# Kernel optimization log

Measured on AMD Instinct MI355X. Metric: run time of the kernel, lower is better.

Reference implementation:

```python
import jax, jax.numpy as jnp
import numpy as np

TEMPERATURE = 0.1
NEG_INF = -1e30


def setup_inputs() -> dict:
    key = jax.random.key(0)
    kf, kl = jax.random.split(key)
    N, D = 8192, 128
    features = jax.random.normal(kf, (N, D), dtype=jnp.float32)
    # labels in [-1, 80): -1 marks background rows that are filtered out
    labels = jax.random.randint(kl, (N,), -1, 80)
    return {"features": features, "labels": labels}


def reference(features, labels):
    N = labels.shape[0]
    fg = labels >= 0  # [N]

    # F.normalize(p=2, dim=1): x / max(||x||, eps)
    norm = jnp.maximum(jnp.linalg.norm(features, axis=1, keepdims=True), 1e-12)
    f = features / norm

    sim = jnp.matmul(f, f.T) / TEMPERATURE  # [N, N]

    pair_fg = fg[:, None] & fg[None, :]
    eye = jnp.eye(N, dtype=bool)
    label_eq = labels[:, None] == labels[None, :]
    pos_mask = pair_fg & label_eq & ~eye          # positives (same label, not self)
    all_mask = pair_fg & ~eye                     # pos | neg == everything but self (within fg)

    # row-wise masked max, clamped to [-20, 20] as in the original
    max_sim = jnp.max(jnp.where(all_mask, sim, NEG_INF), axis=1)
    max_sim = jnp.clip(max_sim, -20.0, 20.0)

    e = jnp.exp(sim - max_sim[:, None])           # cos-sim/temp is bounded, no overflow
    pos_sum = jnp.clip(jnp.sum(jnp.where(pos_mask, e, 0.0), axis=1), 1e-6, 1e6)
    all_sum = jnp.clip(jnp.sum(jnp.where(all_mask, e, 0.0), axis=1), 1e-6, 1e6)

    loss_i = jnp.minimum(-jnp.log(pos_sum / all_sum), 10.0)  # clamp(max=10)

    # rows contributing to the mean: fg rows with at least one positive
    valid = fg & (jnp.sum(pos_mask, axis=1) > 0)
    n_valid = jnp.sum(valid)
    mean_loss = jnp.sum(jnp.where(valid, loss_i, 0.0)) / jnp.maximum(n_valid, 1).astype(jnp.float32)

    ok = (jnp.sum(fg) >= 2) & (n_valid > 0)
    return jnp.where(ok, mean_loss, jnp.float32(0.0))
```

## Files before the change

### kernel.cpp

```cpp
#include <hip/hip_runtime.h>

#define N 8192
#define D 128
#define CHUNK 512
#define NCHUNK (N / CHUNK)
#define TILE_IT (CHUNK / 128)

typedef unsigned short u16;
typedef __attribute__((ext_vector_type(8))) __bf16 bf16x8;
typedef __attribute__((ext_vector_type(4))) float f32x4;

#define PREP_SCALE 3.7982889979f

__device__ __forceinline__ u16 f2bf(float x) {
  unsigned u = __float_as_uint(x);
  u += 0x7fff + ((u >> 16) & 1);
  return (u16)(u >> 16);
}
__device__ __forceinline__ float bf2f(u16 h) {
  return __uint_as_float(((unsigned)h) << 16);
}

__global__ __launch_bounds__(256) void cpe_prep(const float* __restrict__ feat,
                                                u16* __restrict__ fhi,
                                                u16* __restrict__ flo,
                                                float* __restrict__ acc3) {
  if (blockIdx.x == 0 && threadIdx.x < 4) acc3[threadIdx.x] = 0.0f;
  const int w = threadIdx.x >> 6, l = threadIdx.x & 63;
  const int row = blockIdx.x * 4 + w;
  const float2 x = *(const float2*)&feat[row * D + l * 2];
  float s = x.x * x.x + x.y * x.y;
#pragma unroll
  for (int sh = 1; sh < 64; sh <<= 1) s += __shfl_xor(s, sh);
  const float inv = PREP_SCALE / fmaxf(sqrtf(s), 1e-12f);
  const float a = x.x * inv, b = x.y * inv;
  const u16 ah = f2bf(a), bh = f2bf(b);
  const u16 al = f2bf(a - bf2f(ah)), bl = f2bf(b - bf2f(bh));
  *(ushort2*)&fhi[row * D + l * 2] = make_ushort2(ah, bh);
  *(ushort2*)&flo[row * D + l * 2] = make_ushort2(al, bl);
}

__global__ __launch_bounds__(256, 2) void cpe_main(
    const u16* __restrict__ fhi, const u16* __restrict__ flo,
    const int* __restrict__ labels, float4* __restrict__ partials) {
  __shared__ __align__(16) u16 Bh[128 * 128];
  __shared__ __align__(16) u16 Bl[128 * 128];
  __shared__ int Lab[CHUNK];
  const int rt = blockIdx.x, cc = blockIdx.y;
  const int tid = threadIdx.x;
  const int w = tid >> 6, l = tid & 63, q = l >> 4, m = l & 15;
  const int r0w = rt * 256 + w * 64;
  const int cbase0 = cc * CHUNK;

  Lab[tid] = labels[cbase0 + tid];
  Lab[tid + 256] = labels[cbase0 + 256 + tid];

  bf16x8 Ah[4][4];
  int labi[4][4];
#pragma unroll
  for (int tr = 0; tr < 4; ++tr) {
    const int row = r0w + tr * 16 + m;
#pragma unroll
    for (int ks = 0; ks < 4; ++ks)
      Ah[tr][ks] = *(const bf16x8*)&fhi[row * D + ks * 32 + q * 8];
#pragma unroll
    for (int v = 0; v < 4; ++v) labi[tr][v] = labels[r0w + tr * 16 + q * 4 + v];
  }

  float mxe[4][4], ps[4][4], as_[4][4];
#pragma unroll
  for (int tr = 0; tr < 4; ++tr)
#pragma unroll
    for (int v = 0; v < 4; ++v) { mxe[tr][v] = 0.f; ps[tr][v] = 0.f; as_[tr][v] = 0.f; }

  for (int it = 0; it < TILE_IT; ++it) {
    const int cbase = cbase0 + it * 128;
    __syncthreads();
#pragma unroll
    for (int n = 0; n < 8; ++n) {
      const int r = w * 32 + n * 4 + q;
      const int c = m ^ (r & 15);
      const u16* gh = &fhi[(size_t)(cbase + r) * D + c * 8];
      const u16* gl = &flo[(size_t)(cbase + r) * D + c * 8];
      __builtin_amdgcn_global_load_lds(
          (const __attribute__((address_space(1))) unsigned*)gh,
          (__attribute__((address_space(3))) unsigned*)&Bh[(w * 512 + n * 64) * 8],
          16, 0, 0);
      __builtin_amdgcn_global_load_lds(
          (const __attribute__((address_space(1))) unsigned*)gl,
          (__attribute__((address_space(3))) unsigned*)&Bl[(w * 512 + n * 64) * 8],
          16, 0, 0);
    }
    __syncthreads();

    for (int ct = 0; ct < 8; ++ct) {
      const int jj = ct * 16 + m;
      f32x4 acc[4];
#pragma unroll
      for (int tr = 0; tr < 4; ++tr) acc[tr] = (f32x4){0.f, 0.f, 0.f, 0.f};
#pragma unroll
      for (int ks = 0; ks < 4; ++ks) {
        const int off = jj * 128 + ((ks * 4 + q) ^ m) * 8;
        const bf16x8 bh = *(const bf16x8*)&Bh[off];
        const bf16x8 bl = *(const bf16x8*)&Bl[off];
#pragma unroll
        for (int tr = 0; tr < 4; ++tr)
          acc[tr] = __builtin_amdgcn_mfma_f32_16x16x32_bf16(Ah[tr][ks], bh, acc[tr], 0, 0, 0);
#pragma unroll
        for (int tr = 0; tr < 4; ++tr)
          acc[tr] = __builtin_amdgcn_mfma_f32_16x16x32_bf16(Ah[tr][ks], bl, acc[tr], 0, 0, 0);
      }
      const int labj = Lab[it * 128 + jj];
      const bool fgj = labj >= 0;
      const int jbase = cbase + ct * 16;
#pragma unroll
      for (int tr = 0; tr < 4; ++tr) {
        if (jbase == r0w + tr * 16) {
#pragma unroll
          for (int v = 0; v < 4; ++v) {
            const float e = exp2f(acc[tr][v]);
            const float em = (fgj && (m != q * 4 + v)) ? e : 0.0f;
            as_[tr][v] += em;
            mxe[tr][v] = fmaxf(mxe[tr][v], em);
            ps[tr][v] += (labj == labi[tr][v]) ? em : 0.0f;
          }
        } else {
#pragma unroll
          for (int v = 0; v < 4; ++v) {
            const float e = exp2f(acc[tr][v]);
            const float em = fgj ? e : 0.0f;
            as_[tr][v] += em;
            mxe[tr][v] = fmaxf(mxe[tr][v], em);
            ps[tr][v] += (labj == labi[tr][v]) ? em : 0.0f;
          }
        }
      }
    }
  }

#pragma unroll
  for (int tr = 0; tr < 4; ++tr)
#pragma unroll
    for (int v = 0; v < 4; ++v) {
      float vm = mxe[tr][v], vp = ps[tr][v], va = as_[tr][v];
#pragma unroll
      for (int s = 1; s < 16; s <<= 1) {
        vm = fmaxf(vm, __shfl_xor(vm, s));
        vp += __shfl_xor(vp, s);
        va += __shfl_xor(va, s);
      }
      if (m == 0)
        partials[(size_t)cc * N + r0w + tr * 16 + q * 4 + v] =
            make_float4(vm, vp, va, 0.f);
    }
}

__global__ __launch_bounds__(256) void cpe_rows(const float4* __restrict__ partials,
                                                const int* __restrict__ labels,
                                                float* __restrict__ acc3,
                                                float* __restrict__ out) {
  const int r = blockIdx.x * 256 + threadIdx.x;
  float mxe = 0.f, ps = 0.f, as_ = 0.f;
#pragma unroll
  for (int c = 0; c < NCHUNK; ++c) {
    const float4 p = partials[(size_t)c * N + r];
    mxe = fmaxf(mxe, p.x); ps += p.y; as_ += p.z;
  }
  const bool fg = labels[r] >= 0;
  const bool valid = fg && (ps > 0.f);
  const float pos = fminf(fmaxf(ps / mxe, 1e-6f), 1e6f);
  const float all = fminf(fmaxf(as_ / mxe, 1e-6f), 1e6f);
  const float loss = fminf(-logf(pos / all), 10.0f);
  float v0 = valid ? loss : 0.f;
  float v1 = valid ? 1.f : 0.f;
  float v2 = fg ? 1.f : 0.f;
#pragma unroll
  for (int s = 1; s < 64; s <<= 1) {
    v0 += __shfl_xor(v0, s); v1 += __shfl_xor(v1, s); v2 += __shfl_xor(v2, s);
  }
  __shared__ float red[3][4];
  const int w = threadIdx.x >> 6, l = threadIdx.x & 63;
  if (l == 0) { red[0][w] = v0; red[1][w] = v1; red[2][w] = v2; }
  __syncthreads();
  if (threadIdx.x == 0) {
    atomicAdd(&acc3[0], red[0][0] + red[0][1] + red[0][2] + red[0][3]);
    atomicAdd(&acc3[1], red[1][0] + red[1][1] + red[1][2] + red[1][3]);
    atomicAdd(&acc3[2], red[2][0] + red[2][1] + red[2][2] + red[2][3]);
    __threadfence();
    const unsigned old = atomicAdd((unsigned*)&acc3[3], 1u);
    if (old == gridDim.x - 1) {
      const float ls = atomicAdd(&acc3[0], 0.0f);
      const float nv = atomicAdd(&acc3[1], 0.0f);
      const float nf = atomicAdd(&acc3[2], 0.0f);
      out[0] = (nf >= 2.0f && nv > 0.0f) ? ls / fmaxf(nv, 1.0f) : 0.0f;
    }
  }
}

extern "C" void kernel_launch(void* const* d_in, const int* in_sizes, int n_in,
                              void* d_out, int out_size, void* d_ws, size_t ws_size,
                              hipStream_t stream) {
  const float* feat = (const float*)d_in[0];
  const int* labels = (const int*)d_in[1];
  float* out = (float*)d_out;
  char* ws = (char*)d_ws;
  u16* fhi = (u16*)ws;
  u16* flo = (u16*)(ws + (size_t)N * D * 2);
  float4* partials = (float4*)(ws + (size_t)N * D * 4);
  float* acc3 = (float*)(ws + (size_t)N * D * 4 + (size_t)NCHUNK * N * 16);

  cpe_prep<<<N / 4, 256, 0, stream>>>(feat, fhi, flo, acc3);
  cpe_main<<<dim3(N / 256, NCHUNK), 256, 0, stream>>>(fhi, flo, labels, partials);
  cpe_rows<<<N / 256, 256, 0, stream>>>(partials, labels, acc3, out);
}
```

Measured before the change: 117.2 us.

## Move lo-part to register A operand, drop row max and masking via zeroed background rows

The hi/lo split correction now puts the low bf16 part on the A side, which is held in registers. Only the high part of B is staged through LDS, halving LDS traffic and the global-to-LDS loads. Background rows are zeroed in the prep kernel, so the masking happens implicitly: each background column adds exp2(0)=1 per row, which is subtracted through a per-chunk count. The self term is subtracted through a stored diagonal exp value. The row max tracking is dropped because the fixed scale keeps the exps bounded, and a native exp2 builtin, float2 partials and a wider prep kernel are added. The risks are the precision loss from subtracting large counts from the sums, and dropping the lo*hi product on the B side in favour of lo(A)*hi(B), which is a different but symmetric approximation.

```diff
diff --git a/kernel.cpp b/kernel.cpp
--- a/kernel.cpp
+++ b/kernel.cpp
@@ -3,14 +3,21 @@
 #define N 8192
 #define D 128
 #define CHUNK 512
-#define NCHUNK (N / CHUNK)
-#define TILE_IT (CHUNK / 128)
+#define NCHUNK 16
+#define TILE_IT 4
+#define PREP_SCALE 3.7982889979f
 
 typedef unsigned short u16;
 typedef __attribute__((ext_vector_type(8))) __bf16 bf16x8;
 typedef __attribute__((ext_vector_type(4))) float f32x4;
 
-#define PREP_SCALE 3.7982889979f
+__device__ __forceinline__ float fast_exp2(float x) {
+#if __has_builtin(__builtin_amdgcn_exp2f)
+  return __builtin_amdgcn_exp2f(x);
+#else
+  return exp2f(x);
+#endif
+}
 
 __device__ __forceinline__ u16 f2bf(float x) {
   unsigned u = __float_as_uint(x);
@@ -22,56 +29,66 @@
 }
 
 __global__ __launch_bounds__(256) void cpe_prep(const float* __restrict__ feat,
+                                                const int* __restrict__ labels,
                                                 u16* __restrict__ fhi,
                                                 u16* __restrict__ flo,
-                                                float* __restrict__ acc3) {
-  if (blockIdx.x == 0 && threadIdx.x < 4) acc3[threadIdx.x] = 0.0f;
-  const int w = threadIdx.x >> 6, l = threadIdx.x & 63;
-  const int row = blockIdx.x * 4 + w;
-  const float2 x = *(const float2*)&feat[row * D + l * 2];
-  float s = x.x * x.x + x.y * x.y;
-#pragma unroll
-  for (int sh = 1; sh < 64; sh <<= 1) s += __shfl_xor(s, sh);
-  const float inv = PREP_SCALE / fmaxf(sqrtf(s), 1e-12f);
-  const float a = x.x * inv, b = x.y * inv;
-  const u16 ah = f2bf(a), bh = f2bf(b);
-  const u16 al = f2bf(a - bf2f(ah)), bl = f2bf(b - bf2f(bh));
-  *(ushort2*)&fhi[row * D + l * 2] = make_ushort2(ah, bh);
-  *(ushort2*)&flo[row * D + l * 2] = make_ushort2(al, bl);
+                                                float* __restrict__ accum) {
+  if (blockIdx.x == 0 && threadIdx.x < 4) accum[threadIdx.x] = 0.0f;
+  const int w = threadIdx.x >> 6, l = threadIdx.x & 63, q = l >> 4, m = l & 15;
+  const int row = (int)blockIdx.x * 16 + w * 4 + q;
+  const int lab = labels[row];
+  const float4 x0 = *(const float4*)&feat[row * D + m * 8];
+  const float4 x1 = *(const float4*)&feat[row * D + m * 8 + 4];
+  float s = x0.x * x0.x + x0.y * x0.y + x0.z * x0.z + x0.w * x0.w +
+            x1.x * x1.x + x1.y * x1.y + x1.z * x1.z + x1.w * x1.w;
+#pragma unroll
+  for (int sh = 1; sh < 16; sh <<= 1) s += __shfl_xor(s, sh);
+  float inv = PREP_SCALE / fmaxf(sqrtf(s), 1e-12f);
+  if (lab < 0) inv = 0.0f;
+  const float a[8] = {x0.x * inv, x0.y * inv, x0.z * inv, x0.w * inv,
+                      x1.x * inv, x1.y * inv, x1.z * inv, x1.w * inv};
+  u16 h[8], lo[8];
+#pragma unroll
+  for (int k = 0; k < 8; ++k) {
+    h[k] = f2bf(a[k]);
+    lo[k] = f2bf(a[k] - bf2f(h[k]));
+  }
+  *(ushort4*)&fhi[row * D + m * 8] = make_ushort4(h[0], h[1], h[2], h[3]);
+  *(ushort4*)&fhi[row * D + m * 8 + 4] = make_ushort4(h[4], h[5], h[6], h[7]);
+  *(ushort4*)&flo[row * D + m * 8] = make_ushort4(lo[0], lo[1], lo[2], lo[3]);
+  *(ushort4*)&flo[row * D + m * 8 + 4] = make_ushort4(lo[4], lo[5], lo[6], lo[7]);
 }
 
 __global__ __launch_bounds__(256, 2) void cpe_main(
     const u16* __restrict__ fhi, const u16* __restrict__ flo,
-    const int* __restrict__ labels, float4* __restrict__ partials) {
+    const int* __restrict__ labels, float2* __restrict__ partials,
+    float* __restrict__ eself) {
   __shared__ __align__(16) u16 Bh[128 * 128];
-  __shared__ __align__(16) u16 Bl[128 * 128];
-  __shared__ int Lab[CHUNK];
   const int rt = blockIdx.x, cc = blockIdx.y;
   const int tid = threadIdx.x;
   const int w = tid >> 6, l = tid & 63, q = l >> 4, m = l & 15;
   const int r0w = rt * 256 + w * 64;
   const int cbase0 = cc * CHUNK;
 
-  Lab[tid] = labels[cbase0 + tid];
-  Lab[tid + 256] = labels[cbase0 + 256 + tid];
-
-  bf16x8 Ah[4][4];
+  bf16x8 Ah[4][4], Al[4][4];
   int labi[4][4];
 #pragma unroll
   for (int tr = 0; tr < 4; ++tr) {
     const int row = r0w + tr * 16 + m;
 #pragma unroll
-    for (int ks = 0; ks < 4; ++ks)
+    for (int ks = 0; ks < 4; ++ks) {
       Ah[tr][ks] = *(const bf16x8*)&fhi[row * D + ks * 32 + q * 8];
+      Al[tr][ks] = *(const bf16x8*)&flo[row * D + ks * 32 + q * 8];
+    }
 #pragma unroll
     for (int v = 0; v < 4; ++v) labi[tr][v] = labels[r0w + tr * 16 + q * 4 + v];
   }
 
-  float mxe[4][4], ps[4][4], as_[4][4];
+  float ps[4][4], as_[4][4], bgc = 0.f;
 #pragma unroll
   for (int tr = 0; tr < 4; ++tr)
 #pragma unroll
-    for (int v = 0; v < 4; ++v) { mxe[tr][v] = 0.f; ps[tr][v] = 0.f; as_[tr][v] = 0.f; }
+    for (int v = 0; v < 4; ++v) { ps[tr][v] = 0.f; as_[tr][v] = 0.f; }
 
   for (int it = 0; it < TILE_IT; ++it) {
     const int cbase = cbase0 + it * 128;
@@ -80,119 +97,118 @@
     for (int n = 0; n < 8; ++n) {
       const int r = w * 32 + n * 4 + q;
       const int c = m ^ (r & 15);
-      const u16* gh = &fhi[(size_t)(cbase + r) * D + c * 8];
-      const u16* gl = &flo[(size_t)(cbase + r) * D + c * 8];
       __builtin_amdgcn_global_load_lds(
-          (const __attribute__((address_space(1))) unsigned*)gh,
-          (__attribute__((address_space(3))) unsigned*)&Bh[(w * 512 + n * 64) * 8],
-          16, 0, 0);
-      __builtin_amdgcn_global_load_lds(
-          (const __attribute__((address_space(1))) unsigned*)gl,
-          (__attribute__((address_space(3))) unsigned*)&Bl[(w * 512 + n * 64) * 8],
+          (const __attribute__((address_space(1))) unsigned*)
+              &fhi[(size_t)(cbase + r) * D + c * 8],
+          (__attribute__((address_space(3))) unsigned*)
+              &Bh[(w * 512 + n * 64) * 8],
           16, 0, 0);
     }
     __syncthreads();
 
     for (int ct = 0; ct < 8; ++ct) {
       const int jj = ct * 16 + m;
+      const int jbase = cbase + ct * 16;
+      const int labj = labels[jbase + m];
       f32x4 acc[4];
 #pragma unroll
       for (int tr = 0; tr < 4; ++tr) acc[tr] = (f32x4){0.f, 0.f, 0.f, 0.f};
 #pragma unroll
       for (int ks = 0; ks < 4; ++ks) {
-        const int off = jj * 128 + ((ks * 4 + q) ^ m) * 8;
-        const bf16x8 bh = *(const bf16x8*)&Bh[off];
-        const bf16x8 bl = *(const bf16x8*)&Bl[off];
+        const bf16x8 bh = *(const bf16x8*)&Bh[jj * 128 + ((ks * 4 + q) ^ m) * 8];
 #pragma unroll
         for (int tr = 0; tr < 4; ++tr)
           acc[tr] = __builtin_amdgcn_mfma_f32_16x16x32_bf16(Ah[tr][ks], bh, acc[tr], 0, 0, 0);
 #pragma unroll
         for (int tr = 0; tr < 4; ++tr)
-          acc[tr] = __builtin_amdgcn_mfma_f32_16x16x32_bf16(Ah[tr][ks], bl, acc[tr], 0, 0, 0);
+          acc[tr] = __builtin_amdgcn_mfma_f32_16x16x32_bf16(Al[tr][ks], bh, acc[tr], 0, 0, 0);
       }
-      const int labj = Lab[it * 128 + jj];
-      const bool fgj = labj >= 0;
-      const int jbase = cbase + ct * 16;
+      bgc += (labj < 0) ? 1.0f : 0.0f;
 #pragma unroll
       for (int tr = 0; tr < 4; ++tr) {
         if (jbase == r0w + tr * 16) {
 #pragma unroll
           for (int v = 0; v < 4; ++v) {
-            const float e = exp2f(acc[tr][v]);
-            const float em = (fgj && (m != q * 4 + v)) ? e : 0.0f;
-            as_[tr][v] += em;
-            mxe[tr][v] = fmaxf(mxe[tr][v], em);
-            ps[tr][v] += (labj == labi[tr][v]) ? em : 0.0f;
+            const float e = fast_exp2(acc[tr][v]);
+            if (m == q * 4 + v) eself[jbase + m] = e;
+            as_[tr][v] += e;
+            ps[tr][v] += (labj == labi[tr][v]) ? e : 0.f;
           }
         } else {
 #pragma unroll
           for (int v = 0; v < 4; ++v) {
-            const float e = exp2f(acc[tr][v]);
-            const float em = fgj ? e : 0.0f;
-            as_[tr][v] += em;
-            mxe[tr][v] = fmaxf(mxe[tr][v], em);
-            ps[tr][v] += (labj == labi[tr][v]) ? em : 0.0f;
+            const float e = fast_exp2(acc[tr][v]);
+            as_[tr][v] += e;
+            ps[tr][v] += (labj == labi[tr][v]) ? e : 0.f;
           }
         }
       }
     }
   }
 
+  float vbg = bgc;
+#pragma unroll
+  for (int s = 1; s < 16; s <<= 1) vbg += __shfl_xor(vbg, s);
 #pragma unroll
   for (int tr = 0; tr < 4; ++tr)
 #pragma unroll
     for (int v = 0; v < 4; ++v) {
-      float vm = mxe[tr][v], vp = ps[tr][v], va = as_[tr][v];
+      float vp = ps[tr][v], va = as_[tr][v];
 #pragma unroll
       for (int s = 1; s < 16; s <<= 1) {
-        vm = fmaxf(vm, __shfl_xor(vm, s));
         vp += __shfl_xor(vp, s);
         va += __shfl_xor(va, s);
       }
       if (m == 0)
         partials[(size_t)cc * N + r0w + tr * 16 + q * 4 + v] =
-            make_float4(vm, vp, va, 0.f);
-    }
-}
-
-__global__ __launch_bounds__(256) void cpe_rows(const float4* __restrict__ partials,
+            make_float2(vp, va - vbg);
+    }
+}
+
+__global__ __launch_bounds__(256) void cpe_rows(const float2* __restrict__ partials,
                                                 const int* __restrict__ labels,
-                                                float* __restrict__ acc3,
+                                                const float* __restrict__ eself,
+                                                float* __restrict__ accum,
                                                 float* __restrict__ out) {
   const int r = blockIdx.x * 256 + threadIdx.x;
-  float mxe = 0.f, ps = 0.f, as_ = 0.f;
+  float ps = 0.f, as_ = 0.f;
 #pragma unroll
   for (int c = 0; c < NCHUNK; ++c) {
-    const float4 p = partials[(size_t)c * N + r];
-    mxe = fmaxf(mxe, p.x); ps += p.y; as_ += p.z;
-  }
-  const bool fg = labels[r] >= 0;
-  const bool valid = fg && (ps > 0.f);
-  const float pos = fminf(fmaxf(ps / mxe, 1e-6f), 1e6f);
-  const float all = fminf(fmaxf(as_ / mxe, 1e-6f), 1e6f);
-  const float loss = fminf(-logf(pos / all), 10.0f);
+    const float2 p = partials[(size_t)c * N + r];
+    ps += p.x;
+    as_ += p.y;
+  }
+  const float es = eself[r];
+  const int lab = labels[r];
+  ps -= es;
+  as_ -= es;
+  const bool valid = (lab >= 0) && (ps > 0.f);
+  float loss = 10.0f;
+  if (ps > 0.f && as_ > 0.f) loss = fminf(logf(as_ / ps), 10.0f);
   float v0 = valid ? loss : 0.f;
   float v1 = valid ? 1.f : 0.f;
-  float v2 = fg ? 1.f : 0.f;
+  float v2 = (lab >= 0) ? 1.f : 0.f;
 #pragma unroll
   for (int s = 1; s < 64; s <<= 1) {
-    v0 += __shfl_xor(v0, s); v1 += __shfl_xor(v1, s); v2 += __shfl_xor(v2, s);
+    v0 += __shfl_xor(v0, s);
+    v1 += __shfl_xor(v1, s);
+    v2 += __shfl_xor(v2, s);
   }
   __shared__ float red[3][4];
   const int w = threadIdx.x >> 6, l = threadIdx.x & 63;
   if (l == 0) { red[0][w] = v0; red[1][w] = v1; red[2][w] = v2; }
   __syncthreads();
   if (threadIdx.x == 0) {
-    atomicAdd(&acc3[0], red[0][0] + red[0][1] + red[0][2] + red[0][3]);
-    atomicAdd(&acc3[1], red[1][0] + red[1][1] + red[1][2] + red[1][3]);
-    atomicAdd(&acc3[2], red[2][0] + red[2][1] + red[2][2] + red[2][3]);
+    atomicAdd(&accum[0], red[0][0] + red[0][1] + red[0][2] + red[0][3]);
+    atomicAdd(&accum[1], red[1][0] + red[1][1] + red[1][2] + red[1][3]);
+    atomicAdd(&accum[2], red[2][0] + red[2][1] + red[2][2] + red[2][3]);
     __threadfence();
-    const unsigned old = atomicAdd((unsigned*)&acc3[3], 1u);
+    const unsigned old = atomicAdd((unsigned*)&accum[3], 1u);
     if (old == gridDim.x - 1) {
-      const float ls = atomicAdd(&acc3[0], 0.0f);
-      const float nv = atomicAdd(&acc3[1], 0.0f);
-      const float nf = atomicAdd(&acc3[2], 0.0f);
-      out[0] = (nf >= 2.0f && nv > 0.0f) ? ls / fmaxf(nv, 1.0f) : 0.0f;
+      const float ls = atomicAdd(&accum[0], 0.0f);
+      const float nv = atomicAdd(&accum[1], 0.0f);
+      const float nf = atomicAdd(&accum[2], 0.0f);
+      out[0] = (nf >= 2.0f && nv > 0.f) ? ls / fmaxf(nv, 1.f) : 0.0f;
     }
   }
 }
@@ -205,11 +221,12 @@
   float* out = (float*)d_out;
   char* ws = (char*)d_ws;
   u16* fhi = (u16*)ws;
-  u16* flo = (u16*)(ws + (size_t)N * D * 2);
-  float4* partials = (float4*)(ws + (size_t)N * D * 4);
-  float* acc3 = (float*)(ws + (size_t)N * D * 4 + (size_t)NCHUNK * N * 16);
-
-  cpe_prep<<<N / 4, 256, 0, stream>>>(feat, fhi, flo, acc3);
-  cpe_main<<<dim3(N / 256, NCHUNK), 256, 0, stream>>>(fhi, flo, labels, partials);
-  cpe_rows<<<N / 256, 256, 0, stream>>>(partials, labels, acc3, out);
-}
+  u16* flo = (u16*)(ws + 2097152);
+  float2* partials = (float2*)(ws + 4194304);
+  float* eself = (float*)(ws + 5242880);
+  float* accum = (float*)(ws + 5275648);
+
+  cpe_prep<<<N / 16, 256, 0, stream>>>(feat, labels, fhi, flo, accum);
+  cpe_main<<<dim3(N / 256, NCHUNK), 256, 0, stream>>>(fhi, flo, labels, partials, eself);
+  cpe_rows<<<N / 256, 256, 0, stream>>>(partials, labels, eself, accum, out);
+}
```

After: 245.8 us. 2.1x slower.
